# Optimization experiments

Hardware: AMD Instinct MI355X
Metric: run time of the kernel (lower is better)

Reference implementation:

```python
import jax, jax.numpy as jnp
import numpy as np

HEADS = 8

def setup_inputs() -> dict:
    key = jax.random.key(0)
    ks = jax.random.split(key, 7)
    B, C, H, W = 8, 640, 64, 64
    L, CD = 77, 768
    return {
        "hidden_states": jax.random.normal(ks[0], (B, C, H, W), jnp.float32),
        "encoder_hidden_states": jax.random.normal(ks[1], (B, L, CD), jnp.float32),
        "Wq": jax.random.normal(ks[2], (C, C), jnp.float32) * 0.02,
        "Wk": jax.random.normal(ks[3], (CD, C), jnp.float32) * 0.02,
        "Wv": jax.random.normal(ks[4], (CD, C), jnp.float32) * 0.02,
        "Wo": jax.random.normal(ks[5], (C, C), jnp.float32) * 0.02,
        "bo": jnp.zeros((C,), jnp.float32),
    }

def reference(hidden_states, encoder_hidden_states, Wq, Wk, Wv, Wo, bo):
    B, C, H, W = hidden_states.shape
    N = H * W
    dh = C // HEADS
    scale = 1.0 / jnp.sqrt(jnp.asarray(dh, hidden_states.dtype))
    # (B, C, H, W) -> (B, N, C)
    x = hidden_states.reshape(B, C, N).transpose(0, 2, 1)
    q = (x @ Wq).reshape(B, N, HEADS, dh)
    k = (encoder_hidden_states @ Wk).reshape(B, -1, HEADS, dh)
    v = (encoder_hidden_states @ Wv).reshape(B, -1, HEADS, dh)
    # scores: (B, HEADS, N, L) -- full attention_probs materialized as in the original
    scores = jnp.einsum("bnhd,blhd->bhnl", q, k) * scale
    probs = jax.nn.softmax(scores, axis=-1)
    # saliency capture: mean over heads then over k tokens -> (B, 1, H, W)
    saliency = probs.mean(axis=1).mean(axis=-1).reshape(B, 1, H, W)
    out = jnp.einsum("bhnl,blhd->bnhd", probs, v).reshape(B, N, C)
    out = out @ Wo + bo
    out = out.transpose(0, 2, 1).reshape(B, C, H, W)
    return out, saliency
```

## Files before the change

### kernel.cpp

```cpp
#include <hip/hip_runtime.h>

typedef unsigned short u16;
typedef __bf16 bf16x8 __attribute__((ext_vector_type(8)));
typedef float f32x4 __attribute__((ext_vector_type(4)));
typedef unsigned short u16x8 __attribute__((ext_vector_type(8)));
typedef unsigned short u16x4 __attribute__((ext_vector_type(4)));

#define NB 8
#define NC 640
#define NN 4096
#define NL 77
#define NCD 768
#define NH 8
#define NDH 80

__device__ __forceinline__ u16 f2bf(float f) {
  unsigned u = __builtin_bit_cast(unsigned, f);
  u += 0x7fffu + ((u >> 16) & 1u);
  return (u16)(u >> 16);
}

__device__ __forceinline__ f32x4 mfma16(bf16x8 a, bf16x8 b, f32x4 c) {
  return __builtin_amdgcn_mfma_f32_16x16x32_bf16(a, b, c, 0, 0, 0);
}

__device__ __forceinline__ void gload_lds16(const void* g, void* l) {
  __builtin_amdgcn_global_load_lds(
      (const __attribute__((address_space(1))) void*)g,
      (__attribute__((address_space(3))) void*)l, 16, 0, 0);
}

__global__ __launch_bounds__(256) void k_prep(const float* __restrict__ hs,
                                              const float* __restrict__ ehs,
                                              const float* __restrict__ Wq,
                                              const float* __restrict__ Wk,
                                              const float* __restrict__ Wv,
                                              const float* __restrict__ Wo,
                                              u16* __restrict__ xbf,
                                              u16* __restrict__ wqt,
                                              u16* __restrict__ wot,
                                              u16* __restrict__ kbf,
                                              u16* __restrict__ vtbf,
                                              float* __restrict__ sal) {
  __shared__ __align__(16) char smem[37888];
  const int bid = blockIdx.x;
  const int t = threadIdx.x;

  if (bid < 800) {
    float(*tls)[33] = (float(*)[33])smem;
    const int which = bid / 400;
    const int rem = bid % 400;
    const float* in = which ? Wo : Wq;
    u16* outp = which ? wot : wqt;
    const float scale = which ? 1.0f : 0.11180339887498949f;
    const int n0 = (rem % 20) * 32, k0 = (rem / 20) * 32;
    const int r = t >> 3, c4 = (t & 7) * 4;
    float4 v = *(const float4*)(in + (size_t)(k0 + r) * NC + n0 + c4);
    tls[r][c4 + 0] = v.x; tls[r][c4 + 1] = v.y; tls[r][c4 + 2] = v.z; tls[r][c4 + 3] = v.w;
    __syncthreads();
    u16x4 o;
#pragma unroll
    for (int e = 0; e < 4; ++e) o[e] = f2bf(tls[c4 + e][r] * scale);
    *(u16x4*)(outp + (size_t)(n0 + r) * NC + k0 + c4) = o;
    return;
  }
  if (bid < 1760) {
    const int i = bid - 800;
    const int l = i % 96, cg = i / 96;
    if (l >= NL) {
      if (t < 64) {
        int c = cg * 64 + t;
        int h = c / NDH, d = c % NDH;
#pragma unroll
        for (int b = 0; b < NB; ++b)
          vtbf[(((size_t)(b * NH + h)) * NDH + d) * 96 + l] = 0;
      }
      return;
    }
    float(*es)[NCD] = (float(*)[NCD])smem;
    float(*comb)[64][17] = (float(*)[64][17])(smem + 24576);
#pragma unroll
    for (int j = 0; j < 6; ++j) {
      int idx = (t + j * 256) * 4;
      int b = idx / NCD, k = idx % NCD;
      *(float4*)&es[b][k] = *(const float4*)(ehs + ((size_t)(b * NL + l)) * NCD + k);
    }
    __syncthreads();
    const int col = t & 63, kq = t >> 6;
    const int c = cg * 64 + col;
    float ak[NB], av[NB];
#pragma unroll
    for (int b = 0; b < NB; ++b) { ak[b] = 0.f; av[b] = 0.f; }
    const int kbeg = kq * 192, kend = kbeg + 192;
#pragma unroll 4
    for (int k = kbeg; k < kend; ++k) {
      float wk = Wk[(size_t)k * NC + c];
      float wv = Wv[(size_t)k * NC + c];
#pragma unroll
      for (int b = 0; b < NB; ++b) {
        ak[b] = fmaf(es[b][k], wk, ak[b]);
        av[b] = fmaf(es[b][k], wv, av[b]);
      }
    }
    if (kq) {
#pragma unroll
      for (int b = 0; b < NB; ++b) {
        comb[kq - 1][col][b] = ak[b];
        comb[kq - 1][col][8 + b] = av[b];
      }
    }
    __syncthreads();
    if (kq == 0) {
#pragma unroll
      for (int b = 0; b < NB; ++b) {
#pragma unroll
        for (int q = 0; q < 3; ++q) {
          ak[b] += comb[q][col][b];
          av[b] += comb[q][col][8 + b];
        }
      }
      const int h = c / NDH, d = c % NDH;
#pragma unroll
      for (int b = 0; b < NB; ++b) {
        kbf[(((size_t)(b * NH + h)) * 80 + l) * 80 + d] = f2bf(ak[b]);
        vtbf[(((size_t)(b * NH + h)) * NDH + d) * 96 + l] = f2bf(av[b]);
      }
    }
    return;
  }
  if (bid < 6880) {
    float(*tls)[69] = (float(*)[69])smem;
    const int i = bid - 1760;
    const int n0 = (i % 64) * 64;
    const int c0 = ((i / 64) % 10) * 64;
    const int b = i / 640;
    const int rr = t >> 4;
    const int cc = (t & 15) * 4;
#pragma unroll
    for (int p = 0; p < 4; ++p) {
      int c = p * 16 + rr;
      float4 v = *(const float4*)(hs + ((size_t)(b * NC + c0 + c) << 12) + n0 + cc);
      *(float4*)&tls[c][cc] = v;
    }
    __syncthreads();
#pragma unroll
    for (int p = 0; p < 4; ++p) {
      int n = p * 16 + rr;
      u16x4 o;
#pragma unroll
      for (int e = 0; e < 4; ++e) o[e] = f2bf(tls[cc + e][n]);
      *(u16x4*)(xbf + ((size_t)(b * NN + n0 + n)) * NC + c0 + cc) = o;
    }
    return;
  }
  {
    int i = (bid - 6880) * 256 + t;
    if (i < NB * NN) sal[i] = 1.0f / 77.0f;
  }
}

template <int MODE>
__global__ __launch_bounds__(256) void k_gemm(const u16* __restrict__ A,
                                              const u16* __restrict__ Bw,
                                              const float* __restrict__ bias,
                                              u16* __restrict__ outb,
                                              float* __restrict__ outf) {
  __shared__ __align__(16) u16 sA[128 * 64];
  __shared__ __align__(16) u16 sB[128 * 64];
  const int bid = blockIdx.x;
  const int logical = (bid & 7) * 160 + (bid >> 3);
  const int cb = logical % 5, rb = logical / 5;
  const int r0 = rb * 128, c0 = cb * 128;
  const int t = threadIdx.x;
  const int w = t >> 6, lane = t & 63;
  const int wm = w >> 1, wn = w & 1;
  const int fr = lane & 15, g = lane >> 4;
  const int lr = lane >> 3, ls = lane & 7;
  const int sslot = ls ^ lr;

  f32x4 acc[4][4];
  f32x4 z4 = {0.f, 0.f, 0.f, 0.f};
#pragma unroll
  for (int i = 0; i < 4; ++i)
#pragma unroll
    for (int j = 0; j < 4; ++j) acc[i][j] = z4;

  for (int ks = 0; ks < 10; ++ks) {
    const int k0 = ks * 64;
#pragma unroll
    for (int p = 0; p < 4; ++p) {
      int q = w * 4 + p;
      int row = q * 8 + lr;
      gload_lds16(A + (size_t)(r0 + row) * NC + k0 + sslot * 8, sA + q * 512);
      gload_lds16(Bw + (size_t)(c0 + row) * NC + k0 + sslot * 8, sB + q * 512);
    }
    asm volatile("s_waitcnt vmcnt(0)" ::: "memory");
    __syncthreads();
#pragma unroll
    for (int kk = 0; kk < 2; ++kk) {
      bf16x8 af[4], bfr[4];
#pragma unroll
      for (int mt = 0; mt < 4; ++mt) {
        int row = wm * 64 + mt * 16 + fr;
        af[mt] = *(const bf16x8*)((const char*)sA + row * 128 +
                                  ((kk * 64 + g * 16) ^ ((row & 7) << 4)));
      }
#pragma unroll
      for (int nt = 0; nt < 4; ++nt) {
        int row = wn * 64 + nt * 16 + fr;
        bfr[nt] = *(const bf16x8*)((const char*)sB + row * 128 +
                                   ((kk * 64 + g * 16) ^ ((row & 7) << 4)));
      }
#pragma unroll
      for (int mt = 0; mt < 4; ++mt)
#pragma unroll
        for (int nt = 0; nt < 4; ++nt) {
          if (MODE == 0)
            acc[mt][nt] = mfma16(bfr[nt], af[mt], acc[mt][nt]);
          else
            acc[mt][nt] = mfma16(af[mt], bfr[nt], acc[mt][nt]);
        }
    }
    __syncthreads();
  }
  const int b = r0 >> 12, n0 = r0 & 4095;
  if (MODE == 0) {
#pragma unroll
    for (int mt = 0; mt < 4; ++mt) {
      int n = n0 + wm * 64 + mt * 16 + fr;
#pragma unroll
      for (int nt = 0; nt < 4; ++nt) {
        int cbs = c0 + wn * 64 + nt * 16 + g * 4;
        u16x4 o;
#pragma unroll
        for (int r2 = 0; r2 < 4; ++r2) o[r2] = f2bf(acc[mt][nt][r2]);
        *(u16x4*)(outb + ((size_t)(b * NN + n)) * NC + cbs) = o;
      }
    }
  } else {
#pragma unroll
    for (int mt = 0; mt < 4; ++mt) {
      int n = n0 + wm * 64 + mt * 16 + g * 4;
#pragma unroll
      for (int nt = 0; nt < 4; ++nt) {
        int c = c0 + wn * 64 + nt * 16 + fr;
        float bv = bias[c];
        f32x4 o;
#pragma unroll
        for (int r2 = 0; r2 < 4; ++r2) o[r2] = acc[mt][nt][r2] + bv;
        *(f32x4*)(outf + (((size_t)(b * NC + c)) << 12) + n) = o;
      }
    }
  }
}

__global__ __launch_bounds__(256) void k_attn(const u16* __restrict__ qbf,
                                              const u16* __restrict__ kbf,
                                              const u16* __restrict__ vtbf,
                                              u16* __restrict__ obf) {
  __shared__ __align__(16) u16 sP[4][16][104];
  const int bid = blockIdx.x;
  const int n0 = (bid & 63) * 64, h = (bid >> 6) & 7, b = bid >> 9;
  const int t = threadIdx.x, w = t >> 6, lane = t & 63;
  const int fr = lane & 15, g = lane >> 4;

  const size_t qrow = ((size_t)(b * NN + n0 + w * 16 + fr)) * NC + h * NDH;
  bf16x8 qf[3];
#pragma unroll
  for (int kk = 0; kk < 3; ++kk) {
    int d0 = kk * 32 + g * 8;
    bf16x8 v = {};
    if (d0 < NDH) v = *(const bf16x8*)(qbf + qrow + d0);
    qf[kk] = v;
  }
  const size_t kbase = ((size_t)(b * NH + h)) * (80 * 80);
  f32x4 s[5];
  f32x4 z4 = {0.f, 0.f, 0.f, 0.f};
#pragma unroll
  for (int nt = 0; nt < 5; ++nt) s[nt] = z4;
#pragma unroll
  for (int nt = 0; nt < 5; ++nt) {
    const u16* krow = kbf + kbase + (size_t)(nt * 16 + fr) * 80;
#pragma unroll
    for (int kk = 0; kk < 3; ++kk) {
      int d0 = kk * 32 + g * 8;
      bf16x8 kv = {};
      if (d0 < NDH) kv = *(const bf16x8*)(krow + d0);
      s[nt] = mfma16(kv, qf[kk], s[nt]);
    }
  }
  const size_t vbase = ((size_t)(b * NH + h)) * (80 * 96);
  bf16x8 vf[5][3];
#pragma unroll
  for (int nt = 0; nt < 5; ++nt)
#pragma unroll
    for (int kk = 0; kk < 3; ++kk)
      vf[nt][kk] = *(const bf16x8*)(vtbf + vbase + (size_t)(nt * 16 + fr) * 96 +
                                    kk * 32 + g * 8);
  float sum = 0.f;
#pragma unroll
  for (int nt = 0; nt < 5; ++nt)
#pragma unroll
    for (int r = 0; r < 4; ++r) {
      int l = nt * 16 + g * 4 + r;
      float ev = (l < NL) ? __expf(s[nt][r]) : 0.f;
      s[nt][r] = ev;
      sum += ev;
    }
  sum += __shfl_xor(sum, 16);
  sum += __shfl_xor(sum, 32);
  float inv = 1.0f / sum;
#pragma unroll
  for (int nt = 0; nt < 5; ++nt) {
    u16x4 o;
#pragma unroll
    for (int r = 0; r < 4; ++r) o[r] = f2bf(s[nt][r] * inv);
    *(u16x4*)&sP[w][fr][nt * 16 + g * 4] = o;
  }
  __syncthreads();
  bf16x8 ap[3];
#pragma unroll
  for (int kk = 0; kk < 3; ++kk) {
    int l0 = kk * 32 + g * 8;
    bf16x8 v = {};
    if (l0 < 80) v = *(const bf16x8*)&sP[w][fr][l0];
    ap[kk] = v;
  }
  f32x4 o[5];
#pragma unroll
  for (int nt = 0; nt < 5; ++nt) o[nt] = z4;
#pragma unroll
  for (int nt = 0; nt < 5; ++nt)
#pragma unroll
    for (int kk = 0; kk < 3; ++kk)
      o[nt] = mfma16(ap[kk], vf[nt][kk], o[nt]);
#pragma unroll
  for (int nt = 0; nt < 5; ++nt)
#pragma unroll
    for (int r = 0; r < 4; ++r)
      obf[((size_t)(b * NN + n0 + w * 16 + g * 4 + r)) * NC + h * NDH + nt * 16 + fr] =
          f2bf(o[nt][r]);
}

extern "C" void kernel_launch(void* const* d_in, const int* in_sizes, int n_in,
                              void* d_out, int out_size, void* d_ws, size_t ws_size,
                              hipStream_t stream) {
  const float* hs  = (const float*)d_in[0];
  const float* ehs = (const float*)d_in[1];
  const float* Wq  = (const float*)d_in[2];
  const float* Wk  = (const float*)d_in[3];
  const float* Wv  = (const float*)d_in[4];
  const float* Wo  = (const float*)d_in[5];
  const float* bo  = (const float*)d_in[6];
  float* out = (float*)d_out;
  float* sal = out + (size_t)NB * NC * NN;

  u16* ws16 = (u16*)d_ws;
  const size_t xn = (size_t)NB * NN * NC;
  u16* xbf = ws16;
  u16* qbf = ws16 + xn;
  u16* wqt = qbf + xn;
  u16* wot = wqt + (size_t)NC * NC;
  u16* kbf = wot + (size_t)NC * NC;
  u16* vtbf = kbf + (size_t)NB * NH * 80 * 80;
  u16* obf = xbf;

  k_prep<<<7008, 256, 0, stream>>>(hs, ehs, Wq, Wk, Wv, Wo,
                                   xbf, wqt, wot, kbf, vtbf, sal);
  k_gemm<0><<<1280, 256, 0, stream>>>(xbf, wqt, nullptr, qbf, nullptr);
  k_attn<<<NB * NH * 64, 256, 0, stream>>>(qbf, kbf, vtbf, obf);
  k_gemm<1><<<1280, 256, 0, stream>>>(obf, wot, bo, nullptr, out);
}
```

Before: 163.3 us.

## Fuse fp32 hidden-state transpose and bf16 cast into Q-projection GEMM A-operand loads

Drops the prep stage that transposed hidden_states into a bf16 (B,N,C) buffer. The Q GEMM now reads fp32 hidden_states directly from global memory, converts them to bf16 in registers and builds the MFMA A fragments there, so only the weight tile is staged in LDS. This removes a full write and re-read of the 42MB intermediate. In exchange, the A loads become strided scalar fp32 reads that are not staged through LDS or overlapped with compute, and occupancy is tuned with launch_bounds(256,3).

```diff
diff --git a/kernel.cpp b/kernel.cpp
--- a/kernel.cpp
+++ b/kernel.cpp
@@ -30,13 +30,11 @@
       (__attribute__((address_space(3))) void*)l, 16, 0, 0);
 }
 
-__global__ __launch_bounds__(256) void k_prep(const float* __restrict__ hs,
-                                              const float* __restrict__ ehs,
+__global__ __launch_bounds__(256) void k_prep(const float* __restrict__ ehs,
                                               const float* __restrict__ Wq,
                                               const float* __restrict__ Wk,
                                               const float* __restrict__ Wv,
                                               const float* __restrict__ Wo,
-                                              u16* __restrict__ xbf,
                                               u16* __restrict__ wqt,
                                               u16* __restrict__ wot,
                                               u16* __restrict__ kbf,
@@ -128,43 +126,96 @@
     }
     return;
   }
-  if (bid < 6880) {
-    float(*tls)[69] = (float(*)[69])smem;
-    const int i = bid - 1760;
-    const int n0 = (i % 64) * 64;
-    const int c0 = ((i / 64) % 10) * 64;
-    const int b = i / 640;
-    const int rr = t >> 4;
-    const int cc = (t & 15) * 4;
+  {
+    int i = (bid - 1760) * 256 + t;
+    if (i < NB * NN) sal[i] = 1.0f / 77.0f;
+  }
+}
+
+__global__ __launch_bounds__(256, 3) void k_gemm_q(const float* __restrict__ hs,
+                                                   const u16* __restrict__ Bw,
+                                                   u16* __restrict__ outb) {
+  __shared__ __align__(16) u16 sB[128 * 64];
+  const int bid = blockIdx.x;
+  const int logical = (bid & 7) * 160 + (bid >> 3);
+  const int cb = logical % 5, rb = logical / 5;
+  const int r0 = rb * 128, c0 = cb * 128;
+  const int t = threadIdx.x;
+  const int w = t >> 6, lane = t & 63;
+  const int wm = w >> 1, wn = w & 1;
+  const int fr = lane & 15, g = lane >> 4;
+  const int lr = lane >> 3, ls = lane & 7;
+  const int sslot = ls ^ lr;
+  const int b = r0 >> 12, n0 = r0 & 4095;
+  const int nbase = n0 + wm * 64 + fr;
+
+  f32x4 acc[4][4];
+  f32x4 z4 = {0.f, 0.f, 0.f, 0.f};
+#pragma unroll
+  for (int i = 0; i < 4; ++i)
+#pragma unroll
+    for (int j = 0; j < 4; ++j) acc[i][j] = z4;
+
+  for (int ks = 0; ks < 10; ++ks) {
+    const int k0 = ks * 64;
 #pragma unroll
     for (int p = 0; p < 4; ++p) {
-      int c = p * 16 + rr;
-      float4 v = *(const float4*)(hs + ((size_t)(b * NC + c0 + c) << 12) + n0 + cc);
-      *(float4*)&tls[c][cc] = v;
-    }
-    __syncthreads();
-#pragma unroll
-    for (int p = 0; p < 4; ++p) {
-      int n = p * 16 + rr;
+      int q = w * 4 + p;
+      int row = q * 8 + lr;
+      gload_lds16(Bw + (size_t)(c0 + row) * NC + k0 + sslot * 8, sB + q * 512);
+    }
+    bf16x8 af[4][2];
+#pragma unroll
+    for (int kk = 0; kk < 2; ++kk) {
+      const float* hp = hs + (((size_t)(b * NC + k0 + kk * 32 + g * 8)) << 12) + nbase;
+#pragma unroll
+      for (int mt = 0; mt < 4; ++mt) {
+        float tmp[8];
+#pragma unroll
+        for (int j = 0; j < 8; ++j) tmp[j] = hp[((size_t)j << 12) + mt * 16];
+        u16x8 pk;
+#pragma unroll
+        for (int j = 0; j < 8; ++j) pk[j] = f2bf(tmp[j]);
+        af[mt][kk] = __builtin_bit_cast(bf16x8, pk);
+      }
+    }
+    asm volatile("s_waitcnt vmcnt(0)" ::: "memory");
+    __syncthreads();
+#pragma unroll
+    for (int kk = 0; kk < 2; ++kk) {
+      bf16x8 bfr[4];
+#pragma unroll
+      for (int nt = 0; nt < 4; ++nt) {
+        int row = wn * 64 + nt * 16 + fr;
+        bfr[nt] = *(const bf16x8*)((const char*)sB + row * 128 +
+                                   ((kk * 64 + g * 16) ^ ((row & 7) << 4)));
+      }
+#pragma unroll
+      for (int mt = 0; mt < 4; ++mt)
+#pragma unroll
+        for (int nt = 0; nt < 4; ++nt)
+          acc[mt][nt] = mfma16(bfr[nt], af[mt][kk], acc[mt][nt]);
+    }
+    __syncthreads();
+  }
+#pragma unroll
+  for (int mt = 0; mt < 4; ++mt) {
+    int n = n0 + wm * 64 + mt * 16 + fr;
+#pragma unroll
+    for (int nt = 0; nt < 4; ++nt) {
+      int cbs = c0 + wn * 64 + nt * 16 + g * 4;
       u16x4 o;
 #pragma unroll
-      for (int e = 0; e < 4; ++e) o[e] = f2bf(tls[cc + e][n]);
-      *(u16x4*)(xbf + ((size_t)(b * NN + n0 + n)) * NC + c0 + cc) = o;
-    }
-    return;
-  }
-  {
-    int i = (bid - 6880) * 256 + t;
-    if (i < NB * NN) sal[i] = 1.0f / 77.0f;
-  }
-}
-
-template <int MODE>
-__global__ __launch_bounds__(256) void k_gemm(const u16* __restrict__ A,
-                                              const u16* __restrict__ Bw,
-                                              const float* __restrict__ bias,
-                                              u16* __restrict__ outb,
-                                              float* __restrict__ outf) {
+      for (int r2 = 0; r2 < 4; ++r2) o[r2] = f2bf(acc[mt][nt][r2]);
+      *(u16x4*)(outb + ((size_t)(b * NN + n)) * NC + cbs) = o;
+    }
+  }
+}
+
+__global__ __launch_bounds__(256) void k_gemm_o(const u16* __restrict__ A,
+                                                const u16* __restrict__ Bw,
+                                                const float* __restrict__ bias,
+                                                float* __restrict__ outf) {
   __shared__ __align__(16) u16 sA[128 * 64];
   __shared__ __align__(16) u16 sB[128 * 64];
   const int bid = blockIdx.x;
@@ -214,42 +265,23 @@
 #pragma unroll
       for (int mt = 0; mt < 4; ++mt)
 #pragma unroll
-        for (int nt = 0; nt < 4; ++nt) {
-          if (MODE == 0)
-            acc[mt][nt] = mfma16(bfr[nt], af[mt], acc[mt][nt]);
-          else
-            acc[mt][nt] = mfma16(af[mt], bfr[nt], acc[mt][nt]);
-        }
+        for (int nt = 0; nt < 4; ++nt)
+          acc[mt][nt] = mfma16(af[mt], bfr[nt], acc[mt][nt]);
     }
     __syncthreads();
   }
   const int b = r0 >> 12, n0 = r0 & 4095;
-  if (MODE == 0) {
-#pragma unroll
-    for (int mt = 0; mt < 4; ++mt) {
-      int n = n0 + wm * 64 + mt * 16 + fr;
-#pragma unroll
-      for (int nt = 0; nt < 4; ++nt) {
-        int cbs = c0 + wn * 64 + nt * 16 + g * 4;
-        u16x4 o;
-#pragma unroll
-        for (int r2 = 0; r2 < 4; ++r2) o[r2] = f2bf(acc[mt][nt][r2]);
-        *(u16x4*)(outb + ((size_t)(b * NN + n)) * NC + cbs) = o;
-      }
-    }
-  } else {
-#pragma unroll
-    for (int mt = 0; mt < 4; ++mt) {
-      int n = n0 + wm * 64 + mt * 16 + g * 4;
-#pragma unroll
-      for (int nt = 0; nt < 4; ++nt) {
-        int c = c0 + wn * 64 + nt * 16 + fr;
-        float bv = bias[c];
-        f32x4 o;
-#pragma unroll
-        for (int r2 = 0; r2 < 4; ++r2) o[r2] = acc[mt][nt][r2] + bv;
-        *(f32x4*)(outf + (((size_t)(b * NC + c)) << 12) + n) = o;
-      }
+#pragma unroll
+  for (int mt = 0; mt < 4; ++mt) {
+    int n = n0 + wm * 64 + mt * 16 + g * 4;
+#pragma unroll
+    for (int nt = 0; nt < 4; ++nt) {
+      int c = c0 + wn * 64 + nt * 16 + fr;
+      float bv = bias[c];
+      f32x4 o;
+#pragma unroll
+      for (int r2 = 0; r2 < 4; ++r2) o[r2] = acc[mt][nt][r2] + bv;
+      *(f32x4*)(outf + (((size_t)(b * NC + c)) << 12) + n) = o;
     }
   }
 }
@@ -357,17 +389,16 @@
 
   u16* ws16 = (u16*)d_ws;
   const size_t xn = (size_t)NB * NN * NC;
-  u16* xbf = ws16;
+  u16* obf = ws16;
   u16* qbf = ws16 + xn;
   u16* wqt = qbf + xn;
   u16* wot = wqt + (size_t)NC * NC;
   u16* kbf = wot + (size_t)NC * NC;
   u16* vtbf = kbf + (size_t)NB * NH * 80 * 80;
-  u16* obf = xbf;
-
-  k_prep<<<7008, 256, 0, stream>>>(hs, ehs, Wq, Wk, Wv, Wo,
-                                   xbf, wqt, wot, kbf, vtbf, sal);
-  k_gemm<0><<<1280, 256, 0, stream>>>(xbf, wqt, nullptr, qbf, nullptr);
+
+  k_prep<<<1888, 256, 0, stream>>>(ehs, Wq, Wk, Wv, Wo,
+                                   wqt, wot, kbf, vtbf, sal);
+  k_gemm_q<<<1280, 256, 0, stream>>>(hs, wqt, qbf);
   k_attn<<<NB * NH * 64, 256, 0, stream>>>(qbf, kbf, vtbf, obf);
-  k_gemm<1><<<1280, 256, 0, stream>>>(obf, wot, bo, nullptr, out);
-}
+  k_gemm_o<<<1280, 256, 0, stream>>>(obf, wot, bo, out);
+}
```

Measured after the change: 176.2 us. 8.0% more time.

## Double-buffer LDS tiles in k_gemm to overlap global loads with MFMA

Applied to the files above, without the earlier changes.

Adds a second shared-memory buffer for the A and B tiles in the GEMM kernel. The next K-slice is now issued as direct global-to-LDS loads before computing on the current slice, and the wait is partial (vmcnt(8)) so load latency overlaps MFMA work. __syncthreads is replaced with raw s_barrier calls and the K loop is fully unrolled. LDS use doubles to 64KB per block, which may lower occupancy, and skipping the full lgkm wait inside __syncthreads risks ordering issues.

```diff
diff --git a/kernel.cpp b/kernel.cpp
--- a/kernel.cpp
+++ b/kernel.cpp
@@ -165,8 +165,8 @@
                                               const float* __restrict__ bias,
                                               u16* __restrict__ outb,
                                               float* __restrict__ outf) {
-  __shared__ __align__(16) u16 sA[128 * 64];
-  __shared__ __align__(16) u16 sB[128 * 64];
+  __shared__ __align__(16) u16 sA[2][8192];
+  __shared__ __align__(16) u16 sB[2][8192];
   const int bid = blockIdx.x;
   const int logical = (bid & 7) * 160 + (bid >> 3);
   const int cb = logical % 5, rb = logical / 5;
@@ -185,30 +185,44 @@
 #pragma unroll
     for (int j = 0; j < 4; ++j) acc[i][j] = z4;
 
+#define STAGE(kt, buf)                                                               \
+  {                                                                                  \
+    const int k0_ = (kt)*64;                                                         \
+    _Pragma("unroll") for (int p = 0; p < 4; ++p) {                                  \
+      int q = w * 4 + p;                                                             \
+      int row = q * 8 + lr;                                                          \
+      gload_lds16(A + (size_t)(r0 + row) * NC + k0_ + sslot * 8, &sA[(buf)][q * 512]); \
+      gload_lds16(Bw + (size_t)(c0 + row) * NC + k0_ + sslot * 8, &sB[(buf)][q * 512]); \
+    }                                                                                \
+  }
+
+  STAGE(0, 0);
+#pragma unroll
   for (int ks = 0; ks < 10; ++ks) {
-    const int k0 = ks * 64;
-#pragma unroll
-    for (int p = 0; p < 4; ++p) {
-      int q = w * 4 + p;
-      int row = q * 8 + lr;
-      gload_lds16(A + (size_t)(r0 + row) * NC + k0 + sslot * 8, sA + q * 512);
-      gload_lds16(Bw + (size_t)(c0 + row) * NC + k0 + sslot * 8, sB + q * 512);
-    }
-    asm volatile("s_waitcnt vmcnt(0)" ::: "memory");
-    __syncthreads();
+    const int cur = ks & 1;
+    if (ks < 9) {
+      STAGE(ks + 1, cur ^ 1);
+      asm volatile("s_waitcnt vmcnt(8)" ::: "memory");
+    } else {
+      asm volatile("s_waitcnt vmcnt(0)" ::: "memory");
+    }
+    __builtin_amdgcn_s_barrier();
+
+    const char* bA = (const char*)&sA[cur][0];
+    const char* bB = (const char*)&sB[cur][0];
 #pragma unroll
     for (int kk = 0; kk < 2; ++kk) {
       bf16x8 af[4], bfr[4];
 #pragma unroll
       for (int mt = 0; mt < 4; ++mt) {
         int row = wm * 64 + mt * 16 + fr;
-        af[mt] = *(const bf16x8*)((const char*)sA + row * 128 +
+        af[mt] = *(const bf16x8*)(bA + row * 128 +
                                   ((kk * 64 + g * 16) ^ ((row & 7) << 4)));
       }
 #pragma unroll
       for (int nt = 0; nt < 4; ++nt) {
         int row = wn * 64 + nt * 16 + fr;
-        bfr[nt] = *(const bf16x8*)((const char*)sB + row * 128 +
+        bfr[nt] = *(const bf16x8*)(bB + row * 128 +
                                    ((kk * 64 + g * 16) ^ ((row & 7) << 4)));
       }
 #pragma unroll
@@ -221,8 +235,10 @@
             acc[mt][nt] = mfma16(af[mt], bfr[nt], acc[mt][nt]);
         }
     }
-    __syncthreads();
-  }
+    __builtin_amdgcn_s_barrier();
+  }
+#undef STAGE
+
   const int b = r0 >> 12, n0 = r0 & 4095;
   if (MODE == 0) {
 #pragma unroll
```

Result: no change. 165.8 us (+1.6%).
